# Kernel optimization log

Hardware: AMD Instinct MI355X
Metric: run time of the kernel (lower is better)

## Reference

```python
import jax, jax.numpy as jnp
import numpy as np

N_NODES = 50000
N_EDGES = 800000
IN_DIM = 128
E_FEATS = 64
H = 8
D = IN_DIM // H
NEG_SLOPE = 0.2


def setup_inputs() -> dict:
    key = jax.random.key(0)
    ks = jax.random.split(key, 9)
    h = jax.random.normal(ks[0], (N_NODES, IN_DIM), dtype=jnp.float32)
    edge_features = jax.random.normal(ks[1], (N_EDGES, E_FEATS), dtype=jnp.float32)
    src = jax.random.randint(ks[2], (N_EDGES,), 0, N_NODES, dtype=jnp.int32)
    dst = jax.random.randint(ks[3], (N_EDGES,), 0, N_NODES, dtype=jnp.int32)
    s = 0.05
    Wq = jax.random.normal(ks[4], (IN_DIM, IN_DIM), dtype=jnp.float32) * s
    Wk = jax.random.normal(ks[5], (IN_DIM, IN_DIM), dtype=jnp.float32) * s
    Wv = jax.random.normal(ks[6], (IN_DIM, IN_DIM), dtype=jnp.float32) * s
    We = jax.random.normal(ks[7], (H, E_FEATS), dtype=jnp.float32) * s
    Wres = jax.random.normal(ks[8], (IN_DIM, IN_DIM), dtype=jnp.float32) * s
    return {"h": h, "edge_features": edge_features, "src": src, "dst": dst,
            "Wq": Wq, "Wk": Wk, "Wv": Wv, "We": We, "Wres": Wres}


def reference(h, edge_features, src, dst, Wq, Wk, Wv, We, Wres):
    N = h.shape[0]
    # QKV projections (feat_drop is identity at eval)
    q = (h @ Wq.T).reshape(N, H, D)
    k = (h @ Wk.T).reshape(N, H, D)
    v = (h @ Wv.T).reshape(N, H, D)
    # ee / m_att are computed in the original forward but never used (dead code)
    _ee = edge_features @ We.T  # [E, H]

    # v_dot_u('q','k'): dot(q[dst], k[src]) per edge, per head -> [E, H]
    e = jnp.einsum('ehd,ehd->eh', q[dst], k[src])
    e = jnp.where(e >= 0, e, NEG_SLOPE * e)  # leaky_relu

    # edge_softmax over incoming edges of each destination node
    m = jax.ops.segment_max(e, dst, num_segments=N)          # [N, H]
    ex = jnp.exp(e - m[dst])                                 # [E, H]
    z = jax.ops.segment_sum(ex, dst, num_segments=N)         # [N, H]
    alpha = ex / z[dst]                                      # [E, H] (attn_drop identity)

    # weighted aggregation: sum_e alpha * v[src]
    msg = v[src] * alpha[:, :, None]                         # [E, H, D]
    rst = jax.ops.segment_sum(msg, dst, num_segments=N)      # [N, H, D]
    rst = rst.reshape(N, H * D)
    rst = rst + h @ Wres.T                                   # residual
    return rst
```

## Files before the change

### kernel.cpp

```cpp
#include <hip/hip_runtime.h>


#define NEG_SLOPE 0.2f
#define CB 1024

typedef __attribute__((ext_vector_type(8))) short short8;
typedef __attribute__((ext_vector_type(4))) float f32x4;

__device__ __forceinline__ unsigned short f2bf(float f) {
    unsigned int u = __builtin_bit_cast(unsigned int, f);
    u = (u + 0x7fffu + ((u >> 16) & 1u)) >> 16;
    return (unsigned short)u;
}
__device__ __forceinline__ float bf2f(unsigned short s) {
    unsigned int u = (unsigned int)s << 16;
    return __builtin_bit_cast(float, u);
}

__global__ __launch_bounds__(256) void zero_wconv_kernel(
    const float* __restrict__ Wq, const float* __restrict__ Wk,
    const float* __restrict__ Wv, const float* __restrict__ Wres,
    unsigned short* __restrict__ wpk, int* __restrict__ cnt, int n4)
{
    int t = blockIdx.x * 256 + threadIdx.x;
    if (t < 8192) {
        int l = t & 63;
        int v = t >> 6;
        int kk = v & 3;
        int wct = v >> 2;
        int ct = wct & 7;
        int w = wct >> 3;
        const float* W = (w == 0) ? Wq : (w == 1) ? Wk : (w == 2) ? Wv : Wres;
        const float* srcp = W + (size_t)(ct * 16 + (l & 15)) * 128 + kk * 32 + (l >> 4) * 8;
        float4 lo = *reinterpret_cast<const float4*>(srcp);
        float4 hi = *reinterpret_cast<const float4*>(srcp + 4);
        short8 o;
        o[0] = (short)f2bf(lo.x); o[1] = (short)f2bf(lo.y);
        o[2] = (short)f2bf(lo.z); o[3] = (short)f2bf(lo.w);
        o[4] = (short)f2bf(hi.x); o[5] = (short)f2bf(hi.y);
        o[6] = (short)f2bf(hi.z); o[7] = (short)f2bf(hi.w);
        *reinterpret_cast<short8*>(wpk + (size_t)t * 8) = o;
    } else {
        int u = t - 8192;
        if (u < n4) reinterpret_cast<int4*>(cnt)[u] = make_int4(0, 0, 0, 0);
    }
}

__global__ __launch_bounds__(256) void proj_count_kernel(
    const float* __restrict__ h,
    const unsigned short* __restrict__ wpk,
    unsigned short* __restrict__ qb, unsigned int* __restrict__ kvb32,
    unsigned short* __restrict__ resb,
    const int* __restrict__ dst, int* __restrict__ cnt,
    int N, int E, int PB)
{
    if (blockIdx.x >= PB) {
        int start = (blockIdx.x - PB) * 256 + threadIdx.x;
        for (int e = start; e < E; e += CB * 256)
            atomicAdd(&cnt[dst[e]], 1);
        return;
    }

    const int wid = threadIdx.x >> 6;
    const int lane = threadIdx.x & 63;
    const int row0 = blockIdx.x * 128 + wid * 32;
    const int r = lane & 15, g = lane >> 4;

    short8 afrag[2][4];
    #pragma unroll
    for (int grp = 0; grp < 2; ++grp) {
        int arow = row0 + grp * 16 + r;
        if (arow >= N) arow = N - 1;
        const float* hrow = h + (size_t)arow * 128 + g * 8;
        #pragma unroll
        for (int kk = 0; kk < 4; ++kk) {
            float4 lo = *reinterpret_cast<const float4*>(hrow + kk * 32);
            float4 hi = *reinterpret_cast<const float4*>(hrow + kk * 32 + 4);
            short8 a;
            a[0] = (short)f2bf(lo.x); a[1] = (short)f2bf(lo.y);
            a[2] = (short)f2bf(lo.z); a[3] = (short)f2bf(lo.w);
            a[4] = (short)f2bf(hi.x); a[5] = (short)f2bf(hi.y);
            a[6] = (short)f2bf(hi.z); a[7] = (short)f2bf(hi.w);
            afrag[grp][kk] = a;
        }
    }

    #pragma unroll
    for (int sec = 0; sec < 2; ++sec) {
        const int w = (sec == 0) ? 0 : 3;
        unsigned short* O = (sec == 0) ? qb : resb;
        #pragma unroll
        for (int ct = 0; ct < 8; ++ct) {
            const unsigned short* bp =
                wpk + ((size_t)((w * 8 + ct) * 4) * 64 + lane) * 8;
            f32x4 acc[2];
            acc[0] = (f32x4)(0.f); acc[1] = (f32x4)(0.f);
            #pragma unroll
            for (int kk = 0; kk < 4; ++kk) {
                short8 bfrag = *reinterpret_cast<const short8*>(bp + (size_t)kk * 512);
                acc[0] = __builtin_amdgcn_mfma_f32_16x16x32_bf16(
                    afrag[0][kk], bfrag, acc[0], 0, 0, 0);
                acc[1] = __builtin_amdgcn_mfma_f32_16x16x32_bf16(
                    afrag[1][kk], bfrag, acc[1], 0, 0, 0);
            }
            #pragma unroll
            for (int grp = 0; grp < 2; ++grp)
                #pragma unroll
                for (int j = 0; j < 4; ++j) {
                    int orow = row0 + grp * 16 + g * 4 + j;
                    if (orow < N)
                        O[(size_t)orow * 128 + ct * 16 + r] = f2bf(acc[grp][j]);
                }
        }
    }

    #pragma unroll
    for (int ct = 0; ct < 8; ++ct) {
        const unsigned short* bp1 =
            wpk + ((size_t)((1 * 8 + ct) * 4) * 64 + lane) * 8;
        const unsigned short* bp2 =
            wpk + ((size_t)((2 * 8 + ct) * 4) * 64 + lane) * 8;
        f32x4 ak[2], av[2];
        ak[0] = (f32x4)(0.f); ak[1] = (f32x4)(0.f);
        av[0] = (f32x4)(0.f); av[1] = (f32x4)(0.f);
        #pragma unroll
        for (int kk = 0; kk < 4; ++kk) {
            short8 b1 = *reinterpret_cast<const short8*>(bp1 + (size_t)kk * 512);
            short8 b2 = *reinterpret_cast<const short8*>(bp2 + (size_t)kk * 512);
            ak[0] = __builtin_amdgcn_mfma_f32_16x16x32_bf16(afrag[0][kk], b1, ak[0], 0, 0, 0);
            ak[1] = __builtin_amdgcn_mfma_f32_16x16x32_bf16(afrag[1][kk], b1, ak[1], 0, 0, 0);
            av[0] = __builtin_amdgcn_mfma_f32_16x16x32_bf16(afrag[0][kk], b2, av[0], 0, 0, 0);
            av[1] = __builtin_amdgcn_mfma_f32_16x16x32_bf16(afrag[1][kk], b2, av[1], 0, 0, 0);
        }
        #pragma unroll
        for (int grp = 0; grp < 2; ++grp)
            #pragma unroll
            for (int j = 0; j < 4; ++j) {
                int orow = row0 + grp * 16 + g * 4 + j;
                if (orow < N) {
                    unsigned int pk = (unsigned int)f2bf(ak[grp][j])
                                    | ((unsigned int)f2bf(av[grp][j]) << 16);
                    kvb32[(size_t)orow * 128 + ct * 16 + r] = pk;
                }
            }
    }
}

__global__ __launch_bounds__(256) void blocksum_kernel(
    const int* __restrict__ cnt, int* __restrict__ bsum, int N)
{
    __shared__ int ws[4];
    const int tid = threadIdx.x;
    int base = blockIdx.x * 1024 + tid * 4;
    int s = 0;
    if (base + 3 < N) {
        int4 v = *reinterpret_cast<const int4*>(cnt + base);
        s = v.x + v.y + v.z + v.w;
    } else {
        for (int i = 0; i < 4; ++i)
            if (base + i < N) s += cnt[base + i];
    }
    #pragma unroll
    for (int m = 32; m >= 1; m >>= 1) s += __shfl_xor(s, m, 64);
    if ((tid & 63) == 0) ws[tid >> 6] = s;
    __syncthreads();
    if (tid == 0) bsum[blockIdx.x] = ws[0] + ws[1] + ws[2] + ws[3];
}

__global__ __launch_bounds__(256) void scanfinal_kernel(
    const int* __restrict__ cnt, const int* __restrict__ bsum,
    int* __restrict__ row_start, int* __restrict__ cursor,
    int N, int E, int NB)
{
    __shared__ int sboff;
    __shared__ int wsum[4];
    const int tid = threadIdx.x, lane = tid & 63, w = tid >> 6;

    if (tid < 64) {
        int v = (tid < NB && tid < blockIdx.x) ? bsum[tid] : 0;
        #pragma unroll
        for (int m = 32; m >= 1; m >>= 1) v += __shfl_xor(v, m, 64);
        if (tid == 0) sboff = v;
    }
    __syncthreads();

    int base = blockIdx.x * 1024 + tid * 4;
    int a0 = 0, a1 = 0, a2 = 0, a3 = 0;
    if (base + 3 < N) {
        int4 v = *reinterpret_cast<const int4*>(cnt + base);
        a0 = v.x; a1 = v.y; a2 = v.z; a3 = v.w;
    } else {
        if (base + 0 < N) a0 = cnt[base + 0];
        if (base + 1 < N) a1 = cnt[base + 1];
        if (base + 2 < N) a2 = cnt[base + 2];
        if (base + 3 < N) a3 = cnt[base + 3];
    }
    const int tsum = a0 + a1 + a2 + a3;
    int v = tsum;
    #pragma unroll
    for (int off = 1; off < 64; off <<= 1) {
        int t = __shfl_up(v, off, 64);
        if (lane >= off) v += t;
    }
    if (lane == 63) wsum[w] = v;
    __syncthreads();
    int woff = 0;
    for (int i = 0; i < w; ++i) woff += wsum[i];
    int run = sboff + woff + v - tsum;

    int r0 = run, r1 = run + a0, r2 = r1 + a1, r3 = r2 + a2;
    if (base + 3 < N) {
        int4 o = make_int4(r0, r1, r2, r3);
        *reinterpret_cast<int4*>(row_start + base) = o;
        *reinterpret_cast<int4*>(cursor + base) = o;
    } else {
        int rr[4] = {r0, r1, r2, r3};
        for (int i = 0; i < 4; ++i)
            if (base + i < N) { row_start[base + i] = rr[i]; cursor[base + i] = rr[i]; }
    }
    if (blockIdx.x == 0 && tid == 0) row_start[N] = E;
}

__global__ __launch_bounds__(256) void scatter_kernel(
    const int* __restrict__ src, const int* __restrict__ dst,
    int* __restrict__ cursor, int* __restrict__ csr_src, int E)
{
    int e = blockIdx.x * 256 + threadIdx.x;
    if (e < E) {
        int d = dst[e];
        int pos = atomicAdd(&cursor[d], 1);
        csr_src[pos] = src[e];
    }
}

__global__ __launch_bounds__(256) void fused_agg_kernel(
    const unsigned short* __restrict__ qb,
    const unsigned short* __restrict__ kvb,
    const unsigned short* __restrict__ resb,
    const int* __restrict__ row_start, const int* __restrict__ csr_src,
    float* __restrict__ rst, int N)
{
    const int lane = threadIdx.x & 63;
    const int j = lane & 31;
    const int half = lane >> 5;
    const int node = blockIdx.x * 4 + (threadIdx.x >> 6);
    if (node >= N) return;

    const int beg = row_start[node];
    const int nE  = row_start[node + 1] - beg;
    const int* cp = csr_src + beg;

    ushort4 qraw = *reinterpret_cast<const ushort4*>(qb + (size_t)node * 128 + 4 * j);
    const float q0 = bf2f(qraw.x), q1 = bf2f(qraw.y),
                q2 = bf2f(qraw.z), q3 = bf2f(qraw.w);

    float zA = 0.f, zB = 0.f;
    float aA0 = 0.f, aA1 = 0.f, aA2 = 0.f, aA3 = 0.f;
    float aB0 = 0.f, aB1 = 0.f, aB2 = 0.f, aB3 = 0.f;

    if (nE > 0) {
        const int last = nE - 1;
        int sa = cp[min(half, last)];
        int sb = cp[min(half + 2, last)];

        for (int i = 0; i < nE; i += 4) {
            const int ii = i + half;
            const float m0 = (ii < nE) ? 1.f : 0.f;
            const float m1 = (ii + 2 < nE) ? 1.f : 0.f;
            const int s0 = sa, s1 = sb;
            sa = cp[min(ii + 4, last)];
            sb = cp[min(ii + 6, last)];

            short8 kv0 = *reinterpret_cast<const short8*>(kvb + (size_t)s0 * 256 + 8 * j);
            short8 kv1 = *reinterpret_cast<const short8*>(kvb + (size_t)s1 * 256 + 8 * j);

            float p0 = q0 * bf2f((unsigned short)kv0[0])
                     + q1 * bf2f((unsigned short)kv0[2])
                     + q2 * bf2f((unsigned short)kv0[4])
                     + q3 * bf2f((unsigned short)kv0[6]);
            float p1 = q0 * bf2f((unsigned short)kv1[0])
                     + q1 * bf2f((unsigned short)kv1[2])
                     + q2 * bf2f((unsigned short)kv1[4])
                     + q3 * bf2f((unsigned short)kv1[6]);
            p0 += __shfl_xor(p0, 1, 64);
            p0 += __shfl_xor(p0, 2, 64);
            p1 += __shfl_xor(p1, 1, 64);
            p1 += __shfl_xor(p1, 2, 64);
            float e0 = (p0 >= 0.f) ? p0 : NEG_SLOPE * p0;
            float e1 = (p1 >= 0.f) ? p1 : NEG_SLOPE * p1;
            e0 = m0 * __expf(e0);
            e1 = m1 * __expf(e1);
            zA += e0;
            zB += e1;
            aA0 = fmaf(e0, bf2f((unsigned short)kv0[1]), aA0);
            aA1 = fmaf(e0, bf2f((unsigned short)kv0[3]), aA1);
            aA2 = fmaf(e0, bf2f((unsigned short)kv0[5]), aA2);
            aA3 = fmaf(e0, bf2f((unsigned short)kv0[7]), aA3);
            aB0 = fmaf(e1, bf2f((unsigned short)kv1[1]), aB0);
            aB1 = fmaf(e1, bf2f((unsigned short)kv1[3]), aB1);
            aB2 = fmaf(e1, bf2f((unsigned short)kv1[5]), aB2);
            aB3 = fmaf(e1, bf2f((unsigned short)kv1[7]), aB3);
        }
    }

    float a0 = aA0 + aB0, a1 = aA1 + aB1, a2 = aA2 + aB2, a3 = aA3 + aB3;
    float z = zA + zB;
    a0 += __shfl_xor(a0, 32, 64);
    a1 += __shfl_xor(a1, 32, 64);
    a2 += __shfl_xor(a2, 32, 64);
    a3 += __shfl_xor(a3, 32, 64);
    z  += __shfl_xor(z, 32, 64);

    if (half == 0) {
        const size_t base = (size_t)node * 128 + 4 * j;
        ushort4 rb = *reinterpret_cast<const ushort4*>(resb + base);
        float inv = (nE > 0) ? 1.f / z : 0.f;
        float4 rv;
        rv.x = fmaf(a0, inv, bf2f(rb.x));
        rv.y = fmaf(a1, inv, bf2f(rb.y));
        rv.z = fmaf(a2, inv, bf2f(rb.z));
        rv.w = fmaf(a3, inv, bf2f(rb.w));
        *reinterpret_cast<float4*>(rst + base) = rv;
    }
}

extern "C" void kernel_launch(void* const* d_in, const int* in_sizes, int n_in,
                              void* d_out, int out_size, void* d_ws, size_t ws_size,
                              hipStream_t stream) {
    const float* h    = (const float*)d_in[0];
    const int*   src  = (const int*)d_in[2];
    const int*   dst  = (const int*)d_in[3];
    const float* Wq   = (const float*)d_in[4];
    const float* Wk   = (const float*)d_in[5];
    const float* Wv   = (const float*)d_in[6];
    const float* Wres = (const float*)d_in[8];
    float* rst = (float*)d_out;

    const int N = in_sizes[0] / 128;
    const int E = in_sizes[2];

    unsigned short* qb   = (unsigned short*)d_ws;
    unsigned short* kvb  = qb + (size_t)N * 128;
    unsigned short* resb = kvb + (size_t)N * 256;
    unsigned short* wpk  = resb + (size_t)N * 128;
    int* cnt       = (int*)(wpk + 4 * 16384);
    int* row_start = cnt + N;
    int* cursor    = row_start + (N + 1);
    int* csr_src   = cursor + N;
    int* bsum      = csr_src + E;

    const int n4 = N / 4;
    const int NB = (N + 1023) / 1024;
    const int PB = (N + 127) / 128;

    zero_wconv_kernel<<<(8192 + n4 + 255) / 256, 256, 0, stream>>>(
        Wq, Wk, Wv, Wres, wpk, cnt, n4);
    proj_count_kernel<<<PB + CB, 256, 0, stream>>>(
        h, wpk, qb, (unsigned int*)kvb, resb, dst, cnt, N, E, PB);
    blocksum_kernel<<<NB, 256, 0, stream>>>(cnt, bsum, N);
    scanfinal_kernel<<<NB, 256, 0, stream>>>(cnt, bsum, row_start, cursor,
                                             N, E, NB);
    scatter_kernel<<<(E + 255) / 256, 256, 0, stream>>>(src, dst, cursor,
                                                        csr_src, E);
    fused_agg_kernel<<<(N + 3) / 4, 256, 0, stream>>>(qb, kvb, resb,
                                                      row_start, csr_src,
                                                      rst, N);
}
```

Before: 175.3 us.

## Quantize V to per-row int8 and split K/V storage for aggregation gather

V projections are quantized to int8 with a per-node absmax scale, and K is stored as a separate bf16 array, so each gathered source node reads 256B of K plus 128B of V plus a scale instead of 512B of interleaved K/V. The aggregation loop dequantizes V by folding the scale into the softmax weight. The CSR source list gets a zeroed 64-entry pad so the index prefetch can drop its clamping. This cuts gather bandwidth in the edge-bound kernel, at the cost of extra quantization error in V and an additional scale load per edge.

```diff
diff --git a/kernel.cpp b/kernel.cpp
--- a/kernel.cpp
+++ b/kernel.cpp
@@ -20,7 +20,8 @@
 __global__ __launch_bounds__(256) void zero_wconv_kernel(
     const float* __restrict__ Wq, const float* __restrict__ Wk,
     const float* __restrict__ Wv, const float* __restrict__ Wres,
-    unsigned short* __restrict__ wpk, int* __restrict__ cnt, int n4)
+    unsigned short* __restrict__ wpk, int* __restrict__ cnt,
+    int* __restrict__ csr_pad, int n4)
 {
     int t = blockIdx.x * 256 + threadIdx.x;
     if (t < 8192) {
@@ -40,6 +41,7 @@
         o[4] = (short)f2bf(hi.x); o[5] = (short)f2bf(hi.y);
         o[6] = (short)f2bf(hi.z); o[7] = (short)f2bf(hi.w);
         *reinterpret_cast<short8*>(wpk + (size_t)t * 8) = o;
+        if (t < 64) csr_pad[t] = 0;
     } else {
         int u = t - 8192;
         if (u < n4) reinterpret_cast<int4*>(cnt)[u] = make_int4(0, 0, 0, 0);
@@ -49,7 +51,8 @@
 __global__ __launch_bounds__(256) void proj_count_kernel(
     const float* __restrict__ h,
     const unsigned short* __restrict__ wpk,
-    unsigned short* __restrict__ qb, unsigned int* __restrict__ kvb32,
+    unsigned short* __restrict__ qb, unsigned short* __restrict__ kb,
+    signed char* __restrict__ vi8, float* __restrict__ vscl,
     unsigned short* __restrict__ resb,
     const int* __restrict__ dst, int* __restrict__ cnt,
     int N, int E, int PB)
@@ -86,9 +89,9 @@
     }
 
     #pragma unroll
-    for (int sec = 0; sec < 2; ++sec) {
-        const int w = (sec == 0) ? 0 : 3;
-        unsigned short* O = (sec == 0) ? qb : resb;
+    for (int sec = 0; sec < 3; ++sec) {
+        const int w = (sec == 0) ? 0 : (sec == 1) ? 1 : 3;
+        unsigned short* O = (sec == 0) ? qb : (sec == 1) ? kb : resb;
         #pragma unroll
         for (int ct = 0; ct < 8; ++ct) {
             const unsigned short* bp =
@@ -114,33 +117,48 @@
         }
     }
 
-    #pragma unroll
-    for (int ct = 0; ct < 8; ++ct) {
-        const unsigned short* bp1 =
-            wpk + ((size_t)((1 * 8 + ct) * 4) * 64 + lane) * 8;
-        const unsigned short* bp2 =
-            wpk + ((size_t)((2 * 8 + ct) * 4) * 64 + lane) * 8;
-        f32x4 ak[2], av[2];
-        ak[0] = (f32x4)(0.f); ak[1] = (f32x4)(0.f);
-        av[0] = (f32x4)(0.f); av[1] = (f32x4)(0.f);
-        #pragma unroll
-        for (int kk = 0; kk < 4; ++kk) {
-            short8 b1 = *reinterpret_cast<const short8*>(bp1 + (size_t)kk * 512);
-            short8 b2 = *reinterpret_cast<const short8*>(bp2 + (size_t)kk * 512);
-            ak[0] = __builtin_amdgcn_mfma_f32_16x16x32_bf16(afrag[0][kk], b1, ak[0], 0, 0, 0);
-            ak[1] = __builtin_amdgcn_mfma_f32_16x16x32_bf16(afrag[1][kk], b1, ak[1], 0, 0, 0);
-            av[0] = __builtin_amdgcn_mfma_f32_16x16x32_bf16(afrag[0][kk], b2, av[0], 0, 0, 0);
-            av[1] = __builtin_amdgcn_mfma_f32_16x16x32_bf16(afrag[1][kk], b2, av[1], 0, 0, 0);
+    {
+        f32x4 av[2][8];
+        #pragma unroll
+        for (int grp = 0; grp < 2; ++grp)
+            #pragma unroll
+            for (int ct = 0; ct < 8; ++ct) av[grp][ct] = (f32x4)(0.f);
+
+        #pragma unroll
+        for (int ct = 0; ct < 8; ++ct) {
+            const unsigned short* bp =
+                wpk + ((size_t)((2 * 8 + ct) * 4) * 64 + lane) * 8;
+            #pragma unroll
+            for (int kk = 0; kk < 4; ++kk) {
+                short8 bfrag = *reinterpret_cast<const short8*>(bp + (size_t)kk * 512);
+                av[0][ct] = __builtin_amdgcn_mfma_f32_16x16x32_bf16(
+                    afrag[0][kk], bfrag, av[0][ct], 0, 0, 0);
+                av[1][ct] = __builtin_amdgcn_mfma_f32_16x16x32_bf16(
+                    afrag[1][kk], bfrag, av[1][ct], 0, 0, 0);
+            }
         }
+
         #pragma unroll
         for (int grp = 0; grp < 2; ++grp)
             #pragma unroll
             for (int j = 0; j < 4; ++j) {
                 int orow = row0 + grp * 16 + g * 4 + j;
+                float m = fabsf(av[grp][0][j]);
+                #pragma unroll
+                for (int ct = 1; ct < 8; ++ct)
+                    m = fmaxf(m, fabsf(av[grp][ct][j]));
+                #pragma unroll
+                for (int s = 1; s < 16; s <<= 1)
+                    m = fmaxf(m, __shfl_xor(m, s, 64));
+                float scale = m * (1.f / 127.f);
+                float inv = (m > 0.f) ? 127.f / m : 0.f;
                 if (orow < N) {
-                    unsigned int pk = (unsigned int)f2bf(ak[grp][j])
-                                    | ((unsigned int)f2bf(av[grp][j]) << 16);
-                    kvb32[(size_t)orow * 128 + ct * 16 + r] = pk;
+                    #pragma unroll
+                    for (int ct = 0; ct < 8; ++ct) {
+                        int qv = (int)rintf(av[grp][ct][j] * inv);
+                        vi8[(size_t)orow * 128 + ct * 16 + r] = (signed char)qv;
+                    }
+                    if (r == 0) vscl[orow] = scale;
                 }
             }
     }
@@ -235,7 +253,9 @@
 
 __global__ __launch_bounds__(256) void fused_agg_kernel(
     const unsigned short* __restrict__ qb,
-    const unsigned short* __restrict__ kvb,
+    const unsigned short* __restrict__ kb,
+    const unsigned int* __restrict__ vi8_32,
+    const float* __restrict__ vscl,
     const unsigned short* __restrict__ resb,
     const int* __restrict__ row_start, const int* __restrict__ csr_src,
     float* __restrict__ rst, int N)
@@ -259,29 +279,28 @@
     float aB0 = 0.f, aB1 = 0.f, aB2 = 0.f, aB3 = 0.f;
 
     if (nE > 0) {
-        const int last = nE - 1;
-        int sa = cp[min(half, last)];
-        int sb = cp[min(half + 2, last)];
+        int sa = cp[half];
+        int sb = cp[half + 2];
 
         for (int i = 0; i < nE; i += 4) {
             const int ii = i + half;
             const float m0 = (ii < nE) ? 1.f : 0.f;
             const float m1 = (ii + 2 < nE) ? 1.f : 0.f;
             const int s0 = sa, s1 = sb;
-            sa = cp[min(ii + 4, last)];
-            sb = cp[min(ii + 6, last)];
-
-            short8 kv0 = *reinterpret_cast<const short8*>(kvb + (size_t)s0 * 256 + 8 * j);
-            short8 kv1 = *reinterpret_cast<const short8*>(kvb + (size_t)s1 * 256 + 8 * j);
-
-            float p0 = q0 * bf2f((unsigned short)kv0[0])
-                     + q1 * bf2f((unsigned short)kv0[2])
-                     + q2 * bf2f((unsigned short)kv0[4])
-                     + q3 * bf2f((unsigned short)kv0[6]);
-            float p1 = q0 * bf2f((unsigned short)kv1[0])
-                     + q1 * bf2f((unsigned short)kv1[2])
-                     + q2 * bf2f((unsigned short)kv1[4])
-                     + q3 * bf2f((unsigned short)kv1[6]);
+            sa = cp[ii + 4];
+            sb = cp[ii + 6];
+
+            ushort4 k0 = *reinterpret_cast<const ushort4*>(kb + (size_t)s0 * 128 + 4 * j);
+            ushort4 k1 = *reinterpret_cast<const ushort4*>(kb + (size_t)s1 * 128 + 4 * j);
+            unsigned int w0 = vi8_32[(size_t)s0 * 32 + j];
+            unsigned int w1 = vi8_32[(size_t)s1 * 32 + j];
+            float sv0 = vscl[s0];
+            float sv1 = vscl[s1];
+
+            float p0 = q0 * bf2f(k0.x) + q1 * bf2f(k0.y)
+                     + q2 * bf2f(k0.z) + q3 * bf2f(k0.w);
+            float p1 = q0 * bf2f(k1.x) + q1 * bf2f(k1.y)
+                     + q2 * bf2f(k1.z) + q3 * bf2f(k1.w);
             p0 += __shfl_xor(p0, 1, 64);
             p0 += __shfl_xor(p0, 2, 64);
             p1 += __shfl_xor(p1, 1, 64);
@@ -292,14 +311,16 @@
             e1 = m1 * __expf(e1);
             zA += e0;
             zB += e1;
-            aA0 = fmaf(e0, bf2f((unsigned short)kv0[1]), aA0);
-            aA1 = fmaf(e0, bf2f((unsigned short)kv0[3]), aA1);
-            aA2 = fmaf(e0, bf2f((unsigned short)kv0[5]), aA2);
-            aA3 = fmaf(e0, bf2f((unsigned short)kv0[7]), aA3);
-            aB0 = fmaf(e1, bf2f((unsigned short)kv1[1]), aB0);
-            aB1 = fmaf(e1, bf2f((unsigned short)kv1[3]), aB1);
-            aB2 = fmaf(e1, bf2f((unsigned short)kv1[5]), aB2);
-            aB3 = fmaf(e1, bf2f((unsigned short)kv1[7]), aB3);
+            const float f0 = e0 * sv0;
+            const float f1 = e1 * sv1;
+            aA0 = fmaf(f0, (float)(signed char)(w0),       aA0);
+            aA1 = fmaf(f0, (float)(signed char)(w0 >> 8),  aA1);
+            aA2 = fmaf(f0, (float)(signed char)(w0 >> 16), aA2);
+            aA3 = fmaf(f0, (float)(signed char)(w0 >> 24), aA3);
+            aB0 = fmaf(f1, (float)(signed char)(w1),       aB0);
+            aB1 = fmaf(f1, (float)(signed char)(w1 >> 8),  aB1);
+            aB2 = fmaf(f1, (float)(signed char)(w1 >> 16), aB2);
+            aB3 = fmaf(f1, (float)(signed char)(w1 >> 24), aB3);
         }
     }
 
@@ -340,29 +361,31 @@
     const int E = in_sizes[2];
 
     unsigned short* qb   = (unsigned short*)d_ws;
-    unsigned short* kvb  = qb + (size_t)N * 128;
-    unsigned short* resb = kvb + (size_t)N * 256;
-    unsigned short* wpk  = resb + (size_t)N * 128;
+    unsigned short* kb   = qb + (size_t)N * 128;
+    unsigned short* resb = kb + (size_t)N * 128;
+    signed char*    vi8  = (signed char*)(resb + (size_t)N * 128);
+    float*          vscl = (float*)(vi8 + (size_t)N * 128);
+    unsigned short* wpk  = (unsigned short*)(vscl + N);
     int* cnt       = (int*)(wpk + 4 * 16384);
     int* row_start = cnt + N;
     int* cursor    = row_start + (N + 1);
     int* csr_src   = cursor + N;
-    int* bsum      = csr_src + E;
+    int* bsum      = csr_src + E + 64;
 
     const int n4 = N / 4;
     const int NB = (N + 1023) / 1024;
     const int PB = (N + 127) / 128;
 
     zero_wconv_kernel<<<(8192 + n4 + 255) / 256, 256, 0, stream>>>(
-        Wq, Wk, Wv, Wres, wpk, cnt, n4);
+        Wq, Wk, Wv, Wres, wpk, cnt, csr_src + E, n4);
     proj_count_kernel<<<PB + CB, 256, 0, stream>>>(
-        h, wpk, qb, (unsigned int*)kvb, resb, dst, cnt, N, E, PB);
+        h, wpk, qb, kb, vi8, vscl, resb, dst, cnt, N, E, PB);
     blocksum_kernel<<<NB, 256, 0, stream>>>(cnt, bsum, N);
     scanfinal_kernel<<<NB, 256, 0, stream>>>(cnt, bsum, row_start, cursor,
                                              N, E, NB);
     scatter_kernel<<<(E + 255) / 256, 256, 0, stream>>>(src, dst, cursor,
                                                         csr_src, E);
-    fused_agg_kernel<<<(N + 3) / 4, 256, 0, stream>>>(qb, kvb, resb,
-                                                      row_start, csr_src,
-                                                      rst, N);
-}
+    fused_agg_kernel<<<(N + 3) / 4, 256, 0, stream>>>(
+        qb, kb, (const unsigned int*)vi8, vscl, resb, row_start, csr_src,
+        rst, N);
+}
```

After: 166.6 us. 5.0% less time.
